# Kernel optimization log

Hardware: AMD Instinct MI355X
Metric: run time of the kernel (lower is better)

The kernel has to match this reference:

```python
import jax, jax.numpy as jnp
import numpy as np

N0, N1, N2 = 409600, 40960, 4096   # source / mid / target node counts per sampled layer
E1, E2 = 409600, 40960             # edges in layer 1 / layer 2
F_IN, F_HID, F_OUT = 512, 256, 128


def setup_inputs() -> dict:
    key = jax.random.key(0)
    ks = jax.random.split(key, 12)
    s = 1.0 / np.sqrt(F_IN)
    s2 = 1.0 / np.sqrt(F_HID)
    return {
        "x": jax.random.normal(ks[0], (N0, F_IN), dtype=jnp.float32),
        "ei1_src": jax.random.randint(ks[1], (E1,), 0, N0),
        "ei1_dst": jax.random.randint(ks[2], (E1,), 0, N1),
        "ei2_src": jax.random.randint(ks[3], (E2,), 0, N1),
        "ei2_dst": jax.random.randint(ks[4], (E2,), 0, N2),
        "W1l": jax.random.uniform(ks[5], (F_IN, F_HID), jnp.float32, -s, s),
        "b1": jax.random.uniform(ks[6], (F_HID,), jnp.float32, -s, s),
        "W1r": jax.random.uniform(ks[7], (F_IN, F_HID), jnp.float32, -s, s),
        "W2l": jax.random.uniform(ks[8], (F_HID, F_OUT), jnp.float32, -s2, s2),
        "b2": jax.random.uniform(ks[9], (F_OUT,), jnp.float32, -s2, s2),
        "W2r": jax.random.uniform(ks[10], (F_HID, F_OUT), jnp.float32, -s2, s2),
    }


def _sage(x_src, src, dst, n_dst, Wl, b, Wr):
    # PyG SAGEConv (mean aggr): out = lin_l(mean_j x_j) + lin_r(x_target)
    msg = x_src[src]                                           # [E, F] gather
    agg = jax.ops.segment_sum(msg, dst, num_segments=n_dst)    # [n_dst, F]
    cnt = jax.ops.segment_sum(jnp.ones((src.shape[0],), x_src.dtype), dst,
                              num_segments=n_dst)
    mean = agg / jnp.maximum(cnt, 1.0)[:, None]
    x_dst = x_src[:n_dst]                                      # targets are first
    return mean @ Wl + b + x_dst @ Wr


def reference(x, ei1_src, ei1_dst, ei2_src, ei2_dst, W1l, b1, W1r, W2l, b2, W2r):
    h = _sage(x, ei1_src, ei1_dst, N1, W1l, b1, W1r)           # [N1, F_HID]
    h = jax.nn.relu(h)                                         # dropout = identity (eval)
    out = _sage(h, ei2_src, ei2_dst, N2, W2l, b2, W2r)         # [N2, F_OUT]
    return out
```

## Files before the change

### kernel.cpp

```cpp
#include <hip/hip_runtime.h>
#include <hip/hip_bf16.h>

#define N0 409600
#define N1 40960
#define N2 4096
#define E1c 409600
#define E2c 40960
#define F_IN 512
#define F_HID 256
#define F_OUT 128

using bf16x8 = __attribute__((ext_vector_type(8))) short;
using f32x4  = __attribute__((ext_vector_type(4))) float;

__device__ __forceinline__ ushort f2bf(float f) {
    union { float f; unsigned u; } v; v.f = f;
    unsigned r = v.u + 0x7fffu + ((v.u >> 16) & 1u);
    return (ushort)(r >> 16);
}
__device__ __forceinline__ float bf2f(ushort b) {
    union { unsigned u; float f; } v; v.u = ((unsigned)b) << 16;
    return v.f;
}

__device__ __forceinline__ void acc_row(const float* rowp, int lane, float* a) {
    const float4* q = (const float4*)rowp + lane * 2;
    float4 u = q[0], v = q[1];
    a[0] += u.x; a[1] += u.y; a[2] += u.z; a[3] += u.w;
    a[4] += v.x; a[5] += v.y; a[6] += v.z; a[7] += v.w;
}
__device__ __forceinline__ void acc_row(const ushort* rowp, int lane, float* a) {
    ushort4 u = ((const ushort4*)rowp)[lane];
    a[0] += bf2f(u.x); a[1] += bf2f(u.y); a[2] += bf2f(u.z); a[3] += bf2f(u.w);
}
__device__ __forceinline__ void stage_ax(const float* g, ushort* l) {
    float4 v = *(const float4*)g;
    ushort4 o;
    o.x = f2bf(v.x); o.y = f2bf(v.y); o.z = f2bf(v.z); o.w = f2bf(v.w);
    *(ushort4*)l = o;
}
__device__ __forceinline__ void stage_ax(const ushort* g, ushort* l) {
    *(ushort4*)l = *(const ushort4*)g;
}

__global__ void k_prep(const int* __restrict__ dst1, int* __restrict__ cnt1,
                       const int* __restrict__ dst2, int* __restrict__ cnt2,
                       const float* __restrict__ W1l, const float* __restrict__ W1r,
                       const float* __restrict__ W2l, const float* __restrict__ W2r,
                       ushort* __restrict__ W1lT, ushort* __restrict__ W1rT,
                       ushort* __restrict__ W2lT, ushort* __restrict__ W2rT) {
    int idx = blockIdx.x * blockDim.x + threadIdx.x;
    if (idx < E1c) atomicAdd(&cnt1[dst1[idx]], 1);
    else if (idx - E1c < E2c) atomicAdd(&cnt2[dst2[idx - E1c]], 1);
    const int S1 = F_IN * F_HID;
    const int S2 = F_HID * F_OUT;
    if (idx < S1) {
        int k = idx / F_HID, n = idx % F_HID;
        W1lT[(size_t)n * F_IN + k] = f2bf(W1l[idx]);
    } else if (idx < 2 * S1) {
        int j = idx - S1;
        int k = j / F_HID, n = j % F_HID;
        W1rT[(size_t)n * F_IN + k] = f2bf(W1r[j]);
    } else if (idx < 2 * S1 + S2) {
        int j = idx - 2 * S1;
        int k = j / F_OUT, n = j % F_OUT;
        W2lT[(size_t)n * F_HID + k] = f2bf(W2l[j]);
    } else if (idx < 2 * S1 + 2 * S2) {
        int j = idx - 2 * S1 - S2;
        int k = j / F_OUT, n = j % F_OUT;
        W2rT[(size_t)n * F_HID + k] = f2bf(W2r[j]);
    }
}

#define NBLK1 (N1 / 1024)
#define NBLK2 (N2 / 1024)

__global__ __launch_bounds__(1024) void k_scanA2(const int* __restrict__ cnt1, int* __restrict__ off1,
                                                 int* __restrict__ bsum1,
                                                 const int* __restrict__ cnt2, int* __restrict__ off2,
                                                 int* __restrict__ bsum2) {
    __shared__ int wsum[16];
    int blk = blockIdx.x;
    const int* cnt; int* off; int* bsum; int lb;
    if (blk < NBLK1) { cnt = cnt1; off = off1; bsum = bsum1; lb = blk; }
    else             { cnt = cnt2; off = off2; bsum = bsum2; lb = blk - NBLK1; }
    int t = threadIdx.x, lane = t & 63, w = t >> 6;
    int i = lb * 1024 + t;
    int v = cnt[i];
    int s = v;
#pragma unroll
    for (int d = 1; d < 64; d <<= 1) {
        int u = __shfl_up(s, d, 64);
        if (lane >= d) s += u;
    }
    if (lane == 63) wsum[w] = s;
    __syncthreads();
    int wpre = 0, total = 0;
#pragma unroll
    for (int j = 0; j < 16; j++) {
        int u = wsum[j];
        if (j < w) wpre += u;
        total += u;
    }
    off[i] = wpre + (s - v);
    if (t == 0) bsum[lb] = total;
}

__global__ __launch_bounds__(1024) void k_scanB2(int* __restrict__ off1, int* __restrict__ cur1,
                                                 const int* __restrict__ bsum1,
                                                 int* __restrict__ off2, int* __restrict__ cur2,
                                                 const int* __restrict__ bsum2) {
    __shared__ int s_pre, s_tot;
    int blk = blockIdx.x;
    int* off; int* cur; const int* bsum; int lb, nblk, n;
    if (blk < NBLK1) { off = off1; cur = cur1; bsum = bsum1; lb = blk;         nblk = NBLK1; n = N1; }
    else             { off = off2; cur = cur2; bsum = bsum2; lb = blk - NBLK1; nblk = NBLK2; n = N2; }
    int t = threadIdx.x;
    if (t < 64) {
        int v = (t < nblk) ? bsum[t] : 0;
        int p = (t < lb) ? v : 0;
        int tt = v;
#pragma unroll
        for (int d = 32; d >= 1; d >>= 1) {
            p  += __shfl_xor(p, d, 64);
            tt += __shfl_xor(tt, d, 64);
        }
        if (t == 0) { s_pre = p; s_tot = tt; }
    }
    __syncthreads();
    int i = lb * 1024 + t;
    int val = off[i] + s_pre;
    off[i] = val;
    cur[i] = val;
    if (lb == 0 && t == 0) off[n] = s_tot;
}

__global__ void k_scatter2(const int* __restrict__ src1, const int* __restrict__ dst1,
                           int* __restrict__ cur1, int* __restrict__ perm1,
                           const int* __restrict__ src2, const int* __restrict__ dst2,
                           int* __restrict__ cur2, int* __restrict__ perm2) {
    int e = blockIdx.x * blockDim.x + threadIdx.x;
    if (e < E1c) {
        int d = dst1[e];
        int pos = atomicAdd(&cur1[d], 1);
        perm1[pos] = src1[e];
    } else {
        int e2 = e - E1c;
        if (e2 < E2c) {
            int d = dst2[e2];
            int pos = atomicAdd(&cur2[d], 1);
            perm2[pos] = src2[e2];
        }
    }
}

template<int BN, int K, int WN, typename TSRC, bool RELU, bool OUTF32>
__global__ __launch_bounds__(256) void k_sage(
    const TSRC* __restrict__ src,
    const int* __restrict__ perm, const int* __restrict__ off,
    const ushort* __restrict__ BlT, const ushort* __restrict__ BrT,
    const float* __restrict__ bias,
    ushort* __restrict__ outb, float* __restrict__ outf)
{
    constexpr int WM = 4 / WN;
    constexpr int MF = 2 / WM;
    constexpr int NF = BN / (WN * 16);
    constexpr int FPL = (sizeof(TSRC) == 4) ? 8 : 4;

    __shared__ ushort Am[32][K + 8];
    __shared__ ushort Bs[BN][40];
    __shared__ ushort Ax[32][40];

    int tid = threadIdx.x;
    int lane = tid & 63;
    int w = tid >> 6;
    int bm = blockIdx.x * 32;

    for (int rr = 0; rr < 8; rr++) {
        int row = w * 8 + rr;
        int d = bm + row;
        int beg = off[d], end = off[d + 1];
        float a[FPL];
#pragma unroll
        for (int j = 0; j < FPL; j++) a[j] = 0.f;
        int e = beg;
        for (; e + 3 < end; e += 4) {
            int s0 = perm[e], s1 = perm[e + 1], s2 = perm[e + 2], s3 = perm[e + 3];
            acc_row(src + (size_t)s0 * K, lane, a);
            acc_row(src + (size_t)s1 * K, lane, a);
            acc_row(src + (size_t)s2 * K, lane, a);
            acc_row(src + (size_t)s3 * K, lane, a);
        }
        for (; e < end; e++) acc_row(src + (size_t)perm[e] * K, lane, a);
        int deg = end - beg;
        float inv = 1.0f / (float)(deg > 0 ? deg : 1);
        if constexpr (FPL == 8) {
            bf16x8 o;
#pragma unroll
            for (int j = 0; j < 8; j++) o[j] = (short)f2bf(a[j] * inv);
            *(bf16x8*)&Am[row][lane * 8] = o;
        } else {
            ushort4 o;
            o.x = f2bf(a[0] * inv); o.y = f2bf(a[1] * inv);
            o.z = f2bf(a[2] * inv); o.w = f2bf(a[3] * inv);
            *(ushort4*)&Am[row][lane * 4] = o;
        }
    }
    __syncthreads();

    int wm = w / WN, wn = w % WN;
    int sr = tid >> 2, sc = (tid & 3) * 8;
    int r0 = lane & 15, kq = (lane >> 4) * 8;
    f32x4 acc[MF][NF];
#pragma unroll
    for (int i = 0; i < MF; i++)
#pragma unroll
        for (int j = 0; j < NF; j++) acc[i][j] = (f32x4){0.f, 0.f, 0.f, 0.f};

#pragma unroll 1
    for (int part = 0; part < 2; ++part) {
        const ushort* __restrict__ B = part ? BrT : BlT;
        for (int k0 = 0; k0 < K; k0 += 32) {
#pragma unroll
            for (int i = 0; i < BN / 64; i++)
                *(bf16x8*)&Bs[sr + i * 64][sc] =
                    *(const bf16x8*)&B[(size_t)(sr + i * 64) * K + k0 + sc];
            if (part) {
                int r = tid >> 3, c = (tid & 7) * 4;
                stage_ax(src + (size_t)(bm + r) * K + k0 + c, &Ax[r][c]);
            }
            __syncthreads();
            bf16x8 af[MF], bfr[NF];
#pragma unroll
            for (int i = 0; i < MF; i++)
                af[i] = part ? *(const bf16x8*)&Ax[wm * (MF * 16) + i * 16 + r0][kq]
                             : *(const bf16x8*)&Am[wm * (MF * 16) + i * 16 + r0][k0 + kq];
#pragma unroll
            for (int j = 0; j < NF; j++)
                bfr[j] = *(const bf16x8*)&Bs[wn * (NF * 16) + j * 16 + r0][kq];
#pragma unroll
            for (int i = 0; i < MF; i++)
#pragma unroll
                for (int j = 0; j < NF; j++)
                    acc[i][j] = __builtin_amdgcn_mfma_f32_16x16x32_bf16(af[i], bfr[j], acc[i][j], 0, 0, 0);
            __syncthreads();
        }
    }

    int cn0 = lane & 15;
    int rq = (lane >> 4) * 4;
#pragma unroll
    for (int i = 0; i < MF; i++) {
#pragma unroll
        for (int j = 0; j < NF; j++) {
            int col = wn * (NF * 16) + j * 16 + cn0;
            float bv = bias[col];
#pragma unroll
            for (int rr = 0; rr < 4; rr++) {
                int row = bm + wm * (MF * 16) + i * 16 + rq + rr;
                float v = acc[i][j][rr] + bv;
                if (RELU) v = fmaxf(v, 0.f);
                if (OUTF32) outf[(size_t)row * BN + col] = v;
                else        outb[(size_t)row * BN + col] = f2bf(v);
            }
        }
    }
}

static inline size_t align256(size_t x) { return (x + 255) & ~(size_t)255; }

extern "C" void kernel_launch(void* const* d_in, const int* in_sizes, int n_in,
                              void* d_out, int out_size, void* d_ws, size_t ws_size,
                              hipStream_t stream) {
    const float* x = (const float*)d_in[0];
    const int* ei1_src = (const int*)d_in[1];
    const int* ei1_dst = (const int*)d_in[2];
    const int* ei2_src = (const int*)d_in[3];
    const int* ei2_dst = (const int*)d_in[4];
    const float* W1l = (const float*)d_in[5];
    const float* b1 = (const float*)d_in[6];
    const float* W1r = (const float*)d_in[7];
    const float* W2l = (const float*)d_in[8];
    const float* b2 = (const float*)d_in[9];
    const float* W2r = (const float*)d_in[10];
    float* out = (float*)d_out;

    char* p = (char*)d_ws;
    size_t o = 0;
    int* cnt1 = (int*)(p + o); o += (size_t)N1 * 4;
    int* cnt2 = (int*)(p + o); o = align256(o + (size_t)N2 * 4);
    int* off1 = (int*)(p + o); o = align256(o + (size_t)(N1 + 1) * 4);
    int* cur1 = (int*)(p + o); o = align256(o + (size_t)N1 * 4);
    int* perm1 = (int*)(p + o); o = align256(o + (size_t)E1c * 4);
    int* off2 = (int*)(p + o); o = align256(o + (size_t)(N2 + 1) * 4);
    int* cur2 = (int*)(p + o); o = align256(o + (size_t)N2 * 4);
    int* perm2 = (int*)(p + o); o = align256(o + (size_t)E2c * 4);
    int* bsum1 = (int*)(p + o); o = align256(o + 64 * 4);
    int* bsum2 = (int*)(p + o); o = align256(o + 64 * 4);
    ushort* h    = (ushort*)(p + o); o = align256(o + (size_t)N1 * F_HID * 2);
    ushort* W1lT = (ushort*)(p + o); o = align256(o + (size_t)F_IN * F_HID * 2);
    ushort* W1rT = (ushort*)(p + o); o = align256(o + (size_t)F_IN * F_HID * 2);
    ushort* W2lT = (ushort*)(p + o); o = align256(o + (size_t)F_HID * F_OUT * 2);
    ushort* W2rT = (ushort*)(p + o); o = align256(o + (size_t)F_HID * F_OUT * 2);

    hipMemsetAsync(cnt1, 0, (size_t)(N1 + N2) * 4, stream);

    {
        int total = E1c + E2c;
        k_prep<<<(total + 255) / 256, 256, 0, stream>>>(
            ei1_dst, cnt1, ei2_dst, cnt2,
            W1l, W1r, W2l, W2r, W1lT, W1rT, W2lT, W2rT);
    }
    k_scanA2<<<NBLK1 + NBLK2, 1024, 0, stream>>>(cnt1, off1, bsum1, cnt2, off2, bsum2);
    k_scanB2<<<NBLK1 + NBLK2, 1024, 0, stream>>>(off1, cur1, bsum1, off2, cur2, bsum2);
    k_scatter2<<<(E1c + E2c + 255) / 256, 256, 0, stream>>>(
        ei1_src, ei1_dst, cur1, perm1, ei2_src, ei2_dst, cur2, perm2);

    k_sage<256, 512, 4, float, true, false><<<N1 / 32, 256, 0, stream>>>(
        x, perm1, off1, W1lT, W1rT, b1, h, nullptr);

    k_sage<128, 256, 2, ushort, false, true><<<N2 / 32, 256, 0, stream>>>(
        h, perm2, off2, W2lT, W2rT, b2, nullptr, out);
}
```

Before: 329.4 us.

## Read weight fragments directly from global memory and split the GEMM phases

Drops the shared-memory staging buffer for the transposed weight tiles. Each wave now loads its bf16 B fragments straight from global memory, where the small weights should stay cached. The aggregated-mean GEMM phase runs without any block barriers, and only the self-feature phase keeps staging through shared memory. It also adds a minimum of 4 blocks per CU to launch_bounds, which lowers LDS use and raises occupancy but risks uncoalesced global loads and register pressure.

```diff
diff --git a/kernel.cpp b/kernel.cpp
--- a/kernel.cpp
+++ b/kernel.cpp
@@ -155,7 +155,7 @@
 }
 
 template<int BN, int K, int WN, typename TSRC, bool RELU, bool OUTF32>
-__global__ __launch_bounds__(256) void k_sage(
+__global__ __launch_bounds__(256, 4) void k_sage(
     const TSRC* __restrict__ src,
     const int* __restrict__ perm, const int* __restrict__ off,
     const ushort* __restrict__ BlT, const ushort* __restrict__ BrT,
@@ -168,7 +168,6 @@
     constexpr int FPL = (sizeof(TSRC) == 4) ? 8 : 4;
 
     __shared__ ushort Am[32][K + 8];
-    __shared__ ushort Bs[BN][40];
     __shared__ ushort Ax[32][40];
 
     int tid = threadIdx.x;
@@ -209,7 +208,6 @@
     __syncthreads();
 
     int wm = w / WN, wn = w % WN;
-    int sr = tid >> 2, sc = (tid & 3) * 8;
     int r0 = lane & 15, kq = (lane >> 4) * 8;
     f32x4 acc[MF][NF];
 #pragma unroll
@@ -217,27 +215,35 @@
 #pragma unroll
         for (int j = 0; j < NF; j++) acc[i][j] = (f32x4){0.f, 0.f, 0.f, 0.f};
 
-#pragma unroll 1
-    for (int part = 0; part < 2; ++part) {
-        const ushort* __restrict__ B = part ? BrT : BlT;
+#pragma unroll 4
+    for (int k0 = 0; k0 < K; k0 += 32) {
+        bf16x8 af[MF], bfr[NF];
+#pragma unroll
+        for (int i = 0; i < MF; i++)
+            af[i] = *(const bf16x8*)&Am[wm * (MF * 16) + i * 16 + r0][k0 + kq];
+#pragma unroll
+        for (int j = 0; j < NF; j++)
+            bfr[j] = *(const bf16x8*)&BlT[(size_t)(wn * (NF * 16) + j * 16 + r0) * K + k0 + kq];
+#pragma unroll
+        for (int i = 0; i < MF; i++)
+#pragma unroll
+            for (int j = 0; j < NF; j++)
+                acc[i][j] = __builtin_amdgcn_mfma_f32_16x16x32_bf16(af[i], bfr[j], acc[i][j], 0, 0, 0);
+    }
+
+    {
+        int srow = tid >> 3;
+        int scol = (tid & 7) * 4;
         for (int k0 = 0; k0 < K; k0 += 32) {
-#pragma unroll
-            for (int i = 0; i < BN / 64; i++)
-                *(bf16x8*)&Bs[sr + i * 64][sc] =
-                    *(const bf16x8*)&B[(size_t)(sr + i * 64) * K + k0 + sc];
-            if (part) {
-                int r = tid >> 3, c = (tid & 7) * 4;
-                stage_ax(src + (size_t)(bm + r) * K + k0 + c, &Ax[r][c]);
-            }
+            stage_ax(src + (size_t)(bm + srow) * K + k0 + scol, &Ax[srow][scol]);
             __syncthreads();
             bf16x8 af[MF], bfr[NF];
 #pragma unroll
             for (int i = 0; i < MF; i++)
-                af[i] = part ? *(const bf16x8*)&Ax[wm * (MF * 16) + i * 16 + r0][kq]
-                             : *(const bf16x8*)&Am[wm * (MF * 16) + i * 16 + r0][k0 + kq];
+                af[i] = *(const bf16x8*)&Ax[wm * (MF * 16) + i * 16 + r0][kq];
 #pragma unroll
             for (int j = 0; j < NF; j++)
-                bfr[j] = *(const bf16x8*)&Bs[wn * (NF * 16) + j * 16 + r0][kq];
+                bfr[j] = *(const bf16x8*)&BrT[(size_t)(wn * (NF * 16) + j * 16 + r0) * K + k0 + kq];
 #pragma unroll
             for (int i = 0; i < MF; i++)
 #pragma unroll
```

Measured after the change: 330.5 us. About the same (+0.3%).
